# Performance work log

Hardware: AMD Instinct MI355X
Metric: run time of the kernel (lower is better)

## Reference

```python
import jax, jax.numpy as jnp
import numpy as np

D = 65
CHUNK = 64
K = 64
SCALE = D ** (-0.5)

def gelu(x):
    return jax.nn.gelu(x, approximate=False)  # torch nn.GELU default is exact erf

def setup_inputs() -> dict:
    key = jax.random.key(0)
    ks = jax.random.split(key, 16)
    B, N = 32, 16384
    s = SCALE
    return {
        "x": jax.random.normal(ks[0], (B, N, D), jnp.float32),
        # query_gen: Linear(D,D) -> GELU -> Linear(D, K*D)
        "Wq1": jax.random.normal(ks[1], (D, D), jnp.float32) * s,
        "bq1": jnp.zeros((D,), jnp.float32),
        "Wq2": jax.random.normal(ks[2], (D, K * D), jnp.float32) * s,
        "bq2": jnp.zeros((K * D,), jnp.float32),
        "Wk": jax.random.normal(ks[3], (D, D), jnp.float32) * s,
        "bk": jnp.zeros((D,), jnp.float32),
        "Wv": jax.random.normal(ks[4], (D, D), jnp.float32) * s,
        "bv": jnp.zeros((D,), jnp.float32),
        "cross_q": jax.random.normal(ks[5], (1, D), jnp.float32) * s,
        "pos_enc": jax.random.normal(ks[6], (1, CHUNK, D), jnp.float32) * s,
        "Wr": jax.random.normal(ks[7], (D, D), jnp.float32) * (1.0 / np.sqrt(D)),
        "br": jnp.zeros((D,), jnp.float32),
        "gamma": jnp.ones((D,), jnp.float32),
        "beta": jnp.zeros((D,), jnp.float32),
    }

def reference(x, Wq1, bq1, Wq2, bq2, Wk, bk, Wv, bv, cross_q, pos_enc, Wr, br, gamma, beta):
    B, N, d = x.shape
    nb = N // CHUNK  # N chosen divisible by CHUNK -> mask is all True, pad branch skipped

    # global average (mask all-ones => plain mean over N)
    gavg = jnp.mean(x, axis=1)  # [B, D]

    # queries: MLP on global average, reshape to [B, K, D], scaled
    q = (gelu(gavg @ Wq1 + bq1) @ Wq2 + bq2).reshape(B, K, d) * SCALE

    # keys / values: Linear + GELU, chunked, + positional encoding per chunk
    keys = gelu(x @ Wk + bk).reshape(B, nb, CHUNK, d) + pos_enc[None]      # [B,nb,C,D]
    values = gelu(x @ Wv + bv).reshape(B, nb, CHUNK, d) + pos_enc[None]    # [B,nb,C,D]

    # block-local attention (mask is all-True, masked_fill is a no-op)
    scores = jnp.einsum('bkd,bncd->bnkc', q, keys) * SCALE                 # [B,nb,K,C]
    w = jax.nn.softmax(scores, axis=-1)                                    # dropout = eval-mode identity
    blk = jnp.einsum('bnkc,bncd->bnkd', w, values)                         # [B,nb,K,D]
    blk = jnp.transpose(blk, (0, 2, 1, 3))                                 # [B,K,nb,D]

    # cross-block attention with a single learned query
    cs = jnp.einsum('d,bknd->bkn', cross_q[0], blk) * SCALE                # [B,K,nb]
    cw = jax.nn.softmax(cs, axis=-1)
    compressed = jnp.einsum('bkn,bknd->bkd', cw, blk)                      # [B,K,D]

    # residual + LayerNorm
    compressed = compressed + (gavg @ Wr + br)[:, None, :]
    mu = jnp.mean(compressed, axis=-1, keepdims=True)
    var = jnp.var(compressed, axis=-1, keepdims=True)
    return (compressed - mu) * jax.lax.rsqrt(var + 1e-5) * gamma + beta
```

## Files before the change

### kernel.cpp

```cpp
#include <hip/hip_runtime.h>
#include <hip/hip_bf16.h>

#define BATCH 32
#define NSEQ  16384
#define DDIM  65
#define CHUNK 64
#define KQ    64
#define NBLK  256
#define SCALE 0.12403473458920847f

typedef __bf16 bf16x8 __attribute__((ext_vector_type(8)));
typedef float  f32x4  __attribute__((ext_vector_type(4)));
#define MFMA16(a, b, c) __builtin_amdgcn_mfma_f32_16x16x32_bf16(a, b, c, 0, 0, 0)

__device__ __forceinline__ float gelu_exact(float v) {
    return 0.5f * v * (1.0f + erff(v * 0.7071067811865476f));
}

__device__ __forceinline__ float gelu_tanh(float x) {
    float x2 = x * x;
    float t  = 0.7978845608028654f * x * fmaf(0.044715f, x2, 1.0f);
    float e  = __expf(2.0f * t);
    float th = 1.0f - 2.0f * __builtin_amdgcn_rcpf(e + 1.0f);
    return 0.5f * x * (1.0f + th);
}

__global__ __launch_bounds__(256) void k_prep(const float* __restrict__ Wk,
                                              const float* __restrict__ Wv,
                                              __bf16* __restrict__ WkT,
                                              __bf16* __restrict__ WvT) {
    int i = blockIdx.x * 256 + threadIdx.x;
    if (i >= 2 * 80 * 64) return;
    int m = i / 5120;
    int j = i - m * 5120;
    int d = j >> 6, e = j & 63;
    const float* W = m ? Wv : Wk;
    __bf16* T = m ? WvT : WkT;
    T[(size_t)d * 64 + e] = (d < DDIM) ? (__bf16)W[e * DDIM + d] : (__bf16)0.0f;
}

__global__ __launch_bounds__(256) void k_gavg(const float* __restrict__ x,
                                              float* __restrict__ partial) {
    const int s = blockIdx.x;
    const int b = blockIdx.y;
    const int tid = threadIdx.x;
    const int w = tid >> 6, lane = tid & 63;
    const float* xb = x + (size_t)b * NSEQ * DDIM;
    const int n0 = s * 256;
    float acc = 0.f, acce = 0.f;
    #pragma unroll 4
    for (int i = 0; i < 64; ++i) {
        const float* row = xb + (size_t)(n0 + w + i * 4) * DDIM;
        acc  += row[lane];
        acce += row[64];
    }
    __shared__ float part[4][DDIM];
    part[w][lane] = acc;
    if (lane == 0) part[w][64] = acce;
    __syncthreads();
    if (tid < DDIM) {
        partial[((size_t)b * 64 + s) * DDIM + tid] =
            part[0][tid] + part[1][tid] + part[2][tid] + part[3][tid];
    }
}

__global__ __launch_bounds__(256) void k_qgen1(const float* __restrict__ partial,
    const float* __restrict__ Wq1, const float* __restrict__ bq1,
    const float* __restrict__ Wr,  const float* __restrict__ br,
    float* __restrict__ h_out, float* __restrict__ r_out) {
    const int b = blockIdx.x, tid = threadIdx.x;
    __shared__ float g[DDIM];
    if (tid < DDIM) {
        float a = 0.f;
        const float* p = partial + (size_t)b * 64 * DDIM + tid;
        #pragma unroll 8
        for (int s = 0; s < 64; ++s) a += p[s * DDIM];
        g[tid] = a * (1.0f / 16384.0f);
    }
    __syncthreads();
    if (tid < DDIM) {
        float a = bq1[tid];
        for (int e = 0; e < DDIM; ++e) a += g[e] * Wq1[e * DDIM + tid];
        h_out[b * DDIM + tid] = gelu_exact(a);
    } else if (tid >= 128 && tid < 128 + DDIM) {
        const int d = tid - 128;
        float a = br[d];
        for (int e = 0; e < DDIM; ++e) a += g[e] * Wr[e * DDIM + d];
        r_out[b * DDIM + d] = a;
    }
}

__global__ __launch_bounds__(256) void k_qgen2(const float* __restrict__ h_in,
    const float* __restrict__ Wq2, const float* __restrict__ bq2,
    __bf16* __restrict__ qbf, float* __restrict__ q64) {
    const int b = blockIdx.y, tid = threadIdx.x;
    const int o = blockIdx.x * 256 + tid;
    __shared__ float h[DDIM];
    if (tid < DDIM) h[tid] = h_in[b * DDIM + tid];
    __syncthreads();
    if (o >= KQ * DDIM) return;
    float a = bq2[o];
    #pragma unroll 13
    for (int e = 0; e < DDIM; ++e) a += h[e] * Wq2[e * (KQ * DDIM) + o];
    a *= SCALE;
    const int k = o / DDIM, d = o - k * DDIM;
    if (d < 64) qbf[(size_t)b * 4096 + k * 64 + d] = (__bf16)a;
    else        q64[b * 64 + k] = a;
}

__global__ __launch_bounds__(256, 5) void k_attn(const float* __restrict__ x,
    const __bf16* __restrict__ qbf, const float* __restrict__ q64,
    const __bf16* __restrict__ WkT, const __bf16* __restrict__ WvT,
    const float* __restrict__ Wk, const float* __restrict__ bkb,
    const float* __restrict__ Wv, const float* __restrict__ bvb,
    const float* __restrict__ pos, const float* __restrict__ cq,
    __bf16* __restrict__ blk_out, float* __restrict__ cs_out) {
    const int nb = blockIdx.x;
    const int b  = blockIdx.y;
    const int tid = threadIdx.x;
    const int lane = tid & 63, w = tid >> 6;
    const int l16 = lane & 15, quad = lane >> 4;

    __shared__ __align__(16) __bf16 xsP[64 * 72];
    __shared__ __align__(16) __bf16 keys[64 * 72];
    __shared__ __align__(16) __bf16 valsT[64 * 72];
    __shared__ float vals64[64];
    __shared__ float xs64[64];

    {
        const int c = tid >> 2, g = tid & 3;
        const float* xrow = x + ((size_t)b * NSEQ + (size_t)nb * CHUNK + c) * DDIM;
        __bf16* dst = xsP + c * 72;
        #pragma unroll
        for (int j = 0; j < 16; ++j)
            dst[g + 4 * j] = (__bf16)xrow[g + 4 * j];
        if (g == 0) xs64[c] = xrow[64];
    }
    __syncthreads();

    {
        const __bf16* arow = xsP + (w * 16 + l16) * 72 + quad * 8;
        bf16x8 a0 = *(const bf16x8*)arow;
        bf16x8 a1 = *(const bf16x8*)(arow + 32);
        f32x4 ak[5], av[5];
        const f32x4 z = {0.f, 0.f, 0.f, 0.f};
        #pragma unroll
        for (int nt = 0; nt < 5; ++nt) {
            const __bf16* bkr = WkT + (nt * 16 + l16) * 64 + quad * 8;
            const __bf16* bvr = WvT + (nt * 16 + l16) * 64 + quad * 8;
            ak[nt] = MFMA16(a0, *(const bf16x8*)bkr, z);
            ak[nt] = MFMA16(a1, *(const bf16x8*)(bkr + 32), ak[nt]);
            av[nt] = MFMA16(a0, *(const bf16x8*)bvr, z);
            av[nt] = MFMA16(a1, *(const bf16x8*)(bvr + 32), av[nt]);
        }
        float xe[4];
        #pragma unroll
        for (int r = 0; r < 4; ++r) xe[r] = xs64[w * 16 + quad * 4 + r];
        #pragma unroll
        for (int nt = 0; nt < 5; ++nt) {
            const int d = nt * 16 + l16;
            if (d <= 64) {
                const float wk64d = Wk[64 * DDIM + d];
                const float wv64d = Wv[64 * DDIM + d];
                const float bkd = bkb[d], bvd = bvb[d];
                #pragma unroll
                for (int r = 0; r < 4; ++r) {
                    const int c = w * 16 + quad * 4 + r;
                    const float pv = pos[c * DDIM + d];
                    const float kvv = gelu_tanh(ak[nt][r] + xe[r] * wk64d + bkd) + pv;
                    const float vvv = gelu_tanh(av[nt][r] + xe[r] * wv64d + bvd) + pv;
                    keys[c * 72 + d] = (__bf16)kvv;
                    if (d < 64) valsT[d * 72 + c] = (__bf16)vvv;
                    else        vals64[c] = vvv;
                }
            }
        }
    }
    __syncthreads();

    float csr[4];
    {
        const __bf16* aq = qbf + (size_t)b * 4096 + (w * 16 + l16) * 64 + quad * 8;
        bf16x8 qa0 = *(const bf16x8*)aq;
        bf16x8 qa1 = *(const bf16x8*)(aq + 32);
        const f32x4 z = {0.f, 0.f, 0.f, 0.f};
        float st[4][4];
        #pragma unroll
        for (int nt = 0; nt < 4; ++nt) {
            const __bf16* kb = keys + (nt * 16 + l16) * 72 + quad * 8;
            f32x4 sacc = MFMA16(qa0, *(const bf16x8*)kb, z);
            sacc = MFMA16(qa1, *(const bf16x8*)(kb + 32), sacc);
            const float k64c = (float)keys[(nt * 16 + l16) * 72 + 64];
            #pragma unroll
            for (int r = 0; r < 4; ++r) st[nt][r] = sacc[r] * SCALE + 0.f * k64c;
            #pragma unroll
            for (int r = 0; r < 4; ++r)
                st[nt][r] = sacc[r];
            #pragma unroll
            for (int r = 0; r < 4; ++r)
                st[nt][r] = fmaf(q64[b * 64 + w * 16 + quad * 4 + r], k64c,
                                 st[nt][r]) * SCALE;
        }
        float mr[4], sum[4], inv[4];
        #pragma unroll
        for (int r = 0; r < 4; ++r) {
            float m = fmaxf(fmaxf(st[0][r], st[1][r]), fmaxf(st[2][r], st[3][r]));
            m = fmaxf(m, __shfl_xor(m, 1));
            m = fmaxf(m, __shfl_xor(m, 2));
            m = fmaxf(m, __shfl_xor(m, 4));
            m = fmaxf(m, __shfl_xor(m, 8));
            mr[r] = m;
            sum[r] = 0.f;
        }
        #pragma unroll
        for (int nt = 0; nt < 4; ++nt)
            #pragma unroll
            for (int r = 0; r < 4; ++r) {
                st[nt][r] = __expf(st[nt][r] - mr[r]);
                sum[r] += st[nt][r];
            }
        #pragma unroll
        for (int r = 0; r < 4; ++r) {
            float s = sum[r];
            s += __shfl_xor(s, 1);
            s += __shfl_xor(s, 2);
            s += __shfl_xor(s, 4);
            s += __shfl_xor(s, 8);
            inv[r] = __builtin_amdgcn_rcpf(s);
        }
        #pragma unroll
        for (int nt = 0; nt < 4; ++nt)
            #pragma unroll
            for (int r = 0; r < 4; ++r)
                xsP[(w * 16 + quad * 4 + r) * 72 + nt * 16 + l16] =
                    (__bf16)(st[nt][r] * inv[r]);
        float v64l[4];
        #pragma unroll
        for (int nt = 0; nt < 4; ++nt) v64l[nt] = vals64[nt * 16 + l16];
        const float cq64 = cq[64];
        #pragma unroll
        for (int r = 0; r < 4; ++r) {
            float o = st[0][r] * v64l[0];
            o = fmaf(st[1][r], v64l[1], o);
            o = fmaf(st[2][r], v64l[2], o);
            o = fmaf(st[3][r], v64l[3], o);
            o += __shfl_xor(o, 1);
            o += __shfl_xor(o, 2);
            o += __shfl_xor(o, 4);
            o += __shfl_xor(o, 8);
            csr[r] = 0.f;
            if (l16 == 0) {
                const float o64 = o * inv[r];
                const int k = w * 16 + quad * 4 + r;
                blk_out[(((size_t)b * KQ + k) * NBLK + nb) * DDIM + 64] =
                    (__bf16)o64;
                csr[r] = o64 * cq64;
            }
        }
    }
    __syncthreads();

    {
        const __bf16* pr = xsP + (w * 16 + l16) * 72 + quad * 8;
        bf16x8 pa0 = *(const bf16x8*)pr;
        bf16x8 pa1 = *(const bf16x8*)(pr + 32);
        const f32x4 z = {0.f, 0.f, 0.f, 0.f};
        #pragma unroll
        for (int nt = 0; nt < 4; ++nt) {
            const __bf16* vb = valsT + (nt * 16 + l16) * 72 + quad * 8;
            f32x4 o = MFMA16(pa0, *(const bf16x8*)vb, z);
            o = MFMA16(pa1, *(const bf16x8*)(vb + 32), o);
            const int d = nt * 16 + l16;
            const float cqd = cq[d];
            #pragma unroll
            for (int r = 0; r < 4; ++r) {
                const int k = w * 16 + quad * 4 + r;
                blk_out[(((size_t)b * KQ + k) * NBLK + nb) * DDIM + d] =
                    (__bf16)o[r];
                csr[r] = fmaf(o[r], cqd, csr[r]);
            }
        }
        #pragma unroll
        for (int r = 0; r < 4; ++r) {
            float v = csr[r];
            v += __shfl_xor(v, 1);
            v += __shfl_xor(v, 2);
            v += __shfl_xor(v, 4);
            v += __shfl_xor(v, 8);
            if (l16 == 0) {
                const int k = w * 16 + quad * 4 + r;
                cs_out[((size_t)b * KQ + k) * NBLK + nb] = v * SCALE;
            }
        }
    }
}

__global__ __launch_bounds__(256) void k_cross(
    const __bf16* __restrict__ blk, const float* __restrict__ cs,
    const float* __restrict__ r, const float* __restrict__ gamma,
    const float* __restrict__ beta, float* __restrict__ out) {
    const int bk_ = blockIdx.x;
    const int b = bk_ >> 6;
    const int tid = threadIdx.x;
    const int w = tid >> 6, lane = tid & 63;

    __shared__ float ew[NBLK];
    __shared__ float red[4][DDIM];
    __shared__ float vv[DDIM];
    __shared__ float wredA[4];
    __shared__ float stats[2];

    const float v = cs[(size_t)bk_ * NBLK + tid];
    float m = v;
    for (int off = 32; off; off >>= 1) m = fmaxf(m, __shfl_down(m, off));
    if (lane == 0) wredA[w] = m;
    __syncthreads();
    m = fmaxf(fmaxf(wredA[0], wredA[1]), fmaxf(wredA[2], wredA[3]));
    const float e = __expf(v - m);
    ew[tid] = e;
    float s = e;
    for (int off = 32; off; off >>= 1) s += __shfl_down(s, off);
    __syncthreads();
    if (lane == 0) wredA[w] = s;
    __syncthreads();
    const float inv = 1.0f / (wredA[0] + wredA[1] + wredA[2] + wredA[3]);

    const __bf16* base = blk + (size_t)bk_ * NBLK * DDIM;
    float acc = 0.f, acce = 0.f;
    #pragma unroll 4
    for (int i = 0; i < 64; ++i) {
        const int n = w + i * 4;
        const __bf16* row = base + n * DDIM;
        const float wgt = ew[n];
        acc  += wgt * (float)row[lane];
        acce += wgt * (float)row[64];
    }
    red[w][lane] = acc;
    if (lane == 0) red[w][64] = acce;
    __syncthreads();
    if (tid < DDIM) {
        vv[tid] = (red[0][tid] + red[1][tid] + red[2][tid] + red[3][tid]) * inv
                  + r[b * DDIM + tid];
    }
    __syncthreads();
    if (tid < 64) {
        float a  = vv[tid] + (tid == 0 ? vv[64] : 0.f);
        float sq = vv[tid] * vv[tid] + (tid == 0 ? vv[64] * vv[64] : 0.f);
        for (int off = 32; off; off >>= 1) {
            a  += __shfl_down(a, off);
            sq += __shfl_down(sq, off);
        }
        if (tid == 0) {
            const float mu  = a * (1.0f / DDIM);
            const float var = sq * (1.0f / DDIM) - mu * mu;
            stats[0] = mu;
            stats[1] = rsqrtf(var + 1e-5f);
        }
    }
    __syncthreads();
    if (tid < DDIM) {
        out[(size_t)bk_ * DDIM + tid] =
            (vv[tid] - stats[0]) * stats[1] * gamma[tid] + beta[tid];
    }
}

extern "C" void kernel_launch(void* const* d_in, const int* in_sizes, int n_in,
                              void* d_out, int out_size, void* d_ws, size_t ws_size,
                              hipStream_t stream) {
    const float* x    = (const float*)d_in[0];
    const float* Wq1  = (const float*)d_in[1];
    const float* bq1  = (const float*)d_in[2];
    const float* Wq2  = (const float*)d_in[3];
    const float* bq2  = (const float*)d_in[4];
    const float* Wk   = (const float*)d_in[5];
    const float* bk   = (const float*)d_in[6];
    const float* Wv   = (const float*)d_in[7];
    const float* bv   = (const float*)d_in[8];
    const float* cq   = (const float*)d_in[9];
    const float* pos  = (const float*)d_in[10];
    const float* Wr   = (const float*)d_in[11];
    const float* br   = (const float*)d_in[12];
    const float* gamma= (const float*)d_in[13];
    const float* beta = (const float*)d_in[14];
    float* out = (float*)d_out;

    char* w8 = (char*)d_ws;
    float*  partial = (float*)w8;
    float*  rres    = (float*)(w8 + 532480);
    float*  q64     = (float*)(w8 + 540800);
    float*  hbuf    = (float*)(w8 + 548992);
    float*  cs      = (float*)(w8 + 557312);
    __bf16* qbf     = (__bf16*)(w8 + 2654464);
    __bf16* WkT     = (__bf16*)(w8 + 2916608);
    __bf16* WvT     = (__bf16*)(w8 + 2926848);
    __bf16* blk     = (__bf16*)(w8 + 2937088);

    k_prep<<<40, 256, 0, stream>>>(Wk, Wv, WkT, WvT);
    k_gavg<<<dim3(64, BATCH), 256, 0, stream>>>(x, partial);
    k_qgen1<<<BATCH, 256, 0, stream>>>(partial, Wq1, bq1, Wr, br, hbuf, rres);
    k_qgen2<<<dim3(17, BATCH), 256, 0, stream>>>(hbuf, Wq2, bq2, qbf, q64);
    k_attn<<<dim3(NBLK, BATCH), 256, 0, stream>>>(x, qbf, q64, WkT, WvT,
                                                  Wk, bk, Wv, bv, pos, cq,
                                                  blk, cs);
    k_cross<<<BATCH * KQ, 256, 0, stream>>>(blk, cs, rres, gamma, beta, out);
}
```

Baseline: 377.6 us.

## Pad block-output layout, vectorize gavg and cross reads, fold weight prep into gavg

```diff
diff --git a/kernel.cpp b/kernel.cpp
--- a/kernel.cpp
+++ b/kernel.cpp
@@ -13,6 +13,10 @@
 typedef float  f32x4  __attribute__((ext_vector_type(4)));
 #define MFMA16(a, b, c) __builtin_amdgcn_mfma_f32_16x16x32_bf16(a, b, c, 0, 0, 0)
 
+#define BLK_ROWSTRIDE 72
+#define BLK_CHUNKSTRIDE (64 * 72)
+#define BLK_BSTRIDE ((size_t)NBLK * 64 * 72)
+
 __device__ __forceinline__ float gelu_exact(float v) {
     return 0.5f * v * (1.0f + erff(v * 0.7071067811865476f));
 }
@@ -25,42 +29,55 @@
     return 0.5f * x * (1.0f + th);
 }
 
-__global__ __launch_bounds__(256) void k_prep(const float* __restrict__ Wk,
+__global__ __launch_bounds__(320) void k_gavg(const float* __restrict__ x,
+                                              float* __restrict__ partial,
+                                              const float* __restrict__ Wk,
                                               const float* __restrict__ Wv,
                                               __bf16* __restrict__ WkT,
                                               __bf16* __restrict__ WvT) {
-    int i = blockIdx.x * 256 + threadIdx.x;
-    if (i >= 2 * 80 * 64) return;
-    int m = i / 5120;
-    int j = i - m * 5120;
-    int d = j >> 6, e = j & 63;
-    const float* W = m ? Wv : Wk;
-    __bf16* T = m ? WvT : WkT;
-    T[(size_t)d * 64 + e] = (d < DDIM) ? (__bf16)W[e * DDIM + d] : (__bf16)0.0f;
-}
-
-__global__ __launch_bounds__(256) void k_gavg(const float* __restrict__ x,
-                                              float* __restrict__ partial) {
+    const int tid = threadIdx.x;
+    if (blockIdx.y == 32) {
+        const int i = blockIdx.x * 320 + tid;
+        const int m = i / 5120;
+        const int j = i - m * 5120;
+        const int d = j >> 6, e = j & 63;
+        const float* W = m ? Wv : Wk;
+        __bf16* T = m ? WvT : WkT;
+        T[(size_t)d * 64 + e] = (d < DDIM) ? (__bf16)W[e * DDIM + d]
+                                           : (__bf16)0.0f;
+        return;
+    }
     const int s = blockIdx.x;
     const int b = blockIdx.y;
-    const int tid = threadIdx.x;
-    const int w = tid >> 6, lane = tid & 63;
-    const float* xb = x + (size_t)b * NSEQ * DDIM;
-    const int n0 = s * 256;
-    float acc = 0.f, acce = 0.f;
-    #pragma unroll 4
-    for (int i = 0; i < 64; ++i) {
-        const float* row = xb + (size_t)(n0 + w + i * 4) * DDIM;
-        acc  += row[lane];
-        acce += row[64];
-    }
-    __shared__ float part[4][DDIM];
-    part[w][lane] = acc;
-    if (lane == 0) part[w][64] = acce;
+    const int g = tid / 65;
+    const int j = tid - g * 65;
+    const bool active = tid < 260;
+    float acc[4] = {0.f, 0.f, 0.f, 0.f};
+    if (active) {
+        const float4* p = (const float4*)(x + (size_t)b * NSEQ * DDIM
+                                            + (size_t)s * 512 * DDIM);
+        #pragma unroll 8
+        for (int it = 0; it < 32; ++it) {
+            const float4 v = p[(it * 4 + g) * 65 + j];
+            acc[0] += v.x; acc[1] += v.y; acc[2] += v.z; acc[3] += v.w;
+        }
+    }
+    __shared__ float lds[4][65][4];
+    if (active) {
+        lds[g][j][0] = acc[0]; lds[g][j][1] = acc[1];
+        lds[g][j][2] = acc[2]; lds[g][j][3] = acc[3];
+    }
     __syncthreads();
     if (tid < DDIM) {
-        partial[((size_t)b * 64 + s) * DDIM + tid] =
-            part[0][tid] + part[1][tid] + part[2][tid] + part[3][tid];
+        float a = 0.f;
+        #pragma unroll
+        for (int rr = 0; rr < 4; ++rr) {
+            const int f = tid + 65 * rr;
+            const int jj = f >> 2, ee = f & 3;
+            a += lds[0][jj][ee] + lds[1][jj][ee]
+               + lds[2][jj][ee] + lds[3][jj][ee];
+        }
+        partial[((size_t)b * 32 + s) * DDIM + tid] = a;
     }
 }
 
@@ -72,9 +89,9 @@
     __shared__ float g[DDIM];
     if (tid < DDIM) {
         float a = 0.f;
-        const float* p = partial + (size_t)b * 64 * DDIM + tid;
+        const float* p = partial + (size_t)b * 32 * DDIM + tid;
         #pragma unroll 8
-        for (int s = 0; s < 64; ++s) a += p[s * DDIM];
+        for (int s = 0; s < 32; ++s) a += p[s * DDIM];
         g[tid] = a * (1.0f / 16384.0f);
     }
     __syncthreads();
@@ -126,6 +143,9 @@
     __shared__ __align__(16) __bf16 valsT[64 * 72];
     __shared__ float vals64[64];
     __shared__ float xs64[64];
+
+    __bf16* blk_row = blk_out + (size_t)b * BLK_BSTRIDE
+                              + (size_t)nb * BLK_CHUNKSTRIDE;
 
     {
         const int c = tid >> 2, g = tid & 3;
@@ -184,6 +204,9 @@
         bf16x8 qa0 = *(const bf16x8*)aq;
         bf16x8 qa1 = *(const bf16x8*)(aq + 32);
         const f32x4 z = {0.f, 0.f, 0.f, 0.f};
+        float q64k[4];
+        #pragma unroll
+        for (int r = 0; r < 4; ++r) q64k[r] = q64[b * 64 + w * 16 + quad * 4 + r];
         float st[4][4];
         #pragma unroll
         for (int nt = 0; nt < 4; ++nt) {
@@ -192,14 +215,8 @@
             sacc = MFMA16(qa1, *(const bf16x8*)(kb + 32), sacc);
             const float k64c = (float)keys[(nt * 16 + l16) * 72 + 64];
             #pragma unroll
-            for (int r = 0; r < 4; ++r) st[nt][r] = sacc[r] * SCALE + 0.f * k64c;
-            #pragma unroll
             for (int r = 0; r < 4; ++r)
-                st[nt][r] = sacc[r];
-            #pragma unroll
-            for (int r = 0; r < 4; ++r)
-                st[nt][r] = fmaf(q64[b * 64 + w * 16 + quad * 4 + r], k64c,
-                                 st[nt][r]) * SCALE;
+                st[nt][r] = fmaf(q64k[r], k64c, sacc[r]) * SCALE;
         }
         float mr[4], sum[4], inv[4];
         #pragma unroll
@@ -252,8 +269,11 @@
             if (l16 == 0) {
                 const float o64 = o * inv[r];
                 const int k = w * 16 + quad * 4 + r;
-                blk_out[(((size_t)b * KQ + k) * NBLK + nb) * DDIM + 64] =
-                    (__bf16)o64;
+                bf16x8 v8;
+                #pragma unroll
+                for (int i2 = 0; i2 < 8; ++i2) v8[i2] = (__bf16)0.0f;
+                v8[0] = (__bf16)o64;
+                *(bf16x8*)(blk_row + k * BLK_ROWSTRIDE + 64) = v8;
                 csr[r] = o64 * cq64;
             }
         }
@@ -275,8 +295,7 @@
             #pragma unroll
             for (int r = 0; r < 4; ++r) {
                 const int k = w * 16 + quad * 4 + r;
-                blk_out[(((size_t)b * KQ + k) * NBLK + nb) * DDIM + d] =
-                    (__bf16)o[r];
+                blk_row[k * BLK_ROWSTRIDE + d] = (__bf16)o[r];
                 csr[r] = fmaf(o[r], cqd, csr[r]);
             }
         }
@@ -297,17 +316,17 @@
 
 __global__ __launch_bounds__(256) void k_cross(
     const __bf16* __restrict__ blk, const float* __restrict__ cs,
-    const float* __restrict__ r, const float* __restrict__ gamma,
+    const float* __restrict__ rres, const float* __restrict__ gamma,
     const float* __restrict__ beta, float* __restrict__ out) {
     const int bk_ = blockIdx.x;
-    const int b = bk_ >> 6;
+    const int b = bk_ >> 6, k = bk_ & 63;
     const int tid = threadIdx.x;
     const int w = tid >> 6, lane = tid & 63;
 
     __shared__ float ew[NBLK];
-    __shared__ float red[4][DDIM];
+    __shared__ float wredA[4];
+    __shared__ float lred[252][8];
     __shared__ float vv[DDIM];
-    __shared__ float wredA[4];
     __shared__ float stats[2];
 
     const float v = cs[(size_t)bk_ * NBLK + tid];
@@ -325,22 +344,33 @@
     __syncthreads();
     const float inv = 1.0f / (wredA[0] + wredA[1] + wredA[2] + wredA[3]);
 
-    const __bf16* base = blk + (size_t)bk_ * NBLK * DDIM;
-    float acc = 0.f, acce = 0.f;
-    #pragma unroll 4
-    for (int i = 0; i < 64; ++i) {
-        const int n = w + i * 4;
-        const __bf16* row = base + n * DDIM;
-        const float wgt = ew[n];
-        acc  += wgt * (float)row[lane];
-        acce += wgt * (float)row[64];
-    }
-    red[w][lane] = acc;
-    if (lane == 0) red[w][64] = acce;
-    __syncthreads();
-    if (tid < DDIM) {
-        vv[tid] = (red[0][tid] + red[1][tid] + red[2][tid] + red[3][tid]) * inv
-                  + r[b * DDIM + tid];
+    const int g = tid / 9, seg = tid - g * 9;
+    float acc[8] = {0.f, 0.f, 0.f, 0.f, 0.f, 0.f, 0.f, 0.f};
+    if (tid < 252) {
+        const __bf16* base = blk + (size_t)b * BLK_BSTRIDE
+                                 + k * BLK_ROWSTRIDE + seg * 8;
+        #pragma unroll 2
+        for (int it = 0; it < 10; ++it) {
+            const int r = it * 28 + g;
+            if (r < NBLK) {
+                bf16x8 vx = *(const bf16x8*)(base + (size_t)r * BLK_CHUNKSTRIDE);
+                const float wg = ew[r];
+                #pragma unroll
+                for (int i2 = 0; i2 < 8; ++i2)
+                    acc[i2] = fmaf(wg, (float)vx[i2], acc[i2]);
+            }
+        }
+        #pragma unroll
+        for (int i2 = 0; i2 < 8; ++i2) lred[tid][i2] = acc[i2];
+    }
+    __syncthreads();
+    if (tid < 72) {
+        const int sg = tid >> 3, i2 = tid & 7;
+        float a = 0.f;
+        #pragma unroll 7
+        for (int gg = 0; gg < 28; ++gg) a += lred[gg * 9 + sg][i2];
+        const int d = sg * 8 + i2;
+        if (d < DDIM) vv[d] = a * inv + rres[b * DDIM + d];
     }
     __syncthreads();
     if (tid < 64) {
@@ -385,18 +415,17 @@
     float* out = (float*)d_out;
 
     char* w8 = (char*)d_ws;
+    __bf16* blk     = (__bf16*)w8;
     float*  partial = (float*)w8;
-    float*  rres    = (float*)(w8 + 532480);
-    float*  q64     = (float*)(w8 + 540800);
-    float*  hbuf    = (float*)(w8 + 548992);
-    float*  cs      = (float*)(w8 + 557312);
-    __bf16* qbf     = (__bf16*)(w8 + 2654464);
-    __bf16* WkT     = (__bf16*)(w8 + 2916608);
-    __bf16* WvT     = (__bf16*)(w8 + 2926848);
-    __bf16* blk     = (__bf16*)(w8 + 2937088);
-
-    k_prep<<<40, 256, 0, stream>>>(Wk, Wv, WkT, WvT);
-    k_gavg<<<dim3(64, BATCH), 256, 0, stream>>>(x, partial);
+    float*  rres    = (float*)(w8 + 75497472);
+    float*  q64     = (float*)(w8 + 75505792);
+    float*  hbuf    = (float*)(w8 + 75513984);
+    float*  cs      = (float*)(w8 + 75522304);
+    __bf16* qbf     = (__bf16*)(w8 + 77619456);
+    __bf16* WkT     = (__bf16*)(w8 + 77881600);
+    __bf16* WvT     = (__bf16*)(w8 + 77891840);
+
+    k_gavg<<<dim3(32, 33), 320, 0, stream>>>(x, partial, Wk, Wv, WkT, WvT);
     k_qgen1<<<BATCH, 256, 0, stream>>>(partial, Wq1, bq1, Wr, br, hbuf, rres);
     k_qgen2<<<dim3(17, BATCH), 256, 0, stream>>>(hbuf, Wq2, bq2, qbf, q64);
     k_attn<<<dim3(NBLK, BATCH), 256, 0, stream>>>(x, qbf, q64, WkT, WvT,
```

After: 378.0 us. Within noise of the previous version (+0.1%).
